# Kernel optimization log

Measured on AMD Instinct MI355X. Metric: run time of the kernel, lower is better.

Reference implementation:

```python
import jax, jax.numpy as jnp
import numpy as np

B, T, D_MODEL = 2, 2048, 2048
N_HEADS, N_KV = 16, 8
HEAD_DIM = D_MODEL // N_HEADS  # 128
EPS = 1e-6


def rmsnorm(x, g):
    # qwen-compatible: compute in fp32, scale by learned weight
    xf = x.astype(jnp.float32)
    var = jnp.mean(xf * xf, axis=-1, keepdims=True)
    return (xf * jax.lax.rsqrt(var + EPS) * g).astype(x.dtype)


def apply_rope(x, cos, sin):
    # x: [b, h, t, d]; cos/sin: [t, d]
    d = x.shape[-1]
    x1, x2 = x[..., : d // 2], x[..., d // 2 :]
    rotated = jnp.concatenate([-x2, x1], axis=-1)
    return x * cos[None, None, :, :] + rotated * sin[None, None, :, :]


def setup_inputs() -> dict:
    key = jax.random.key(0)
    ks = jax.random.split(key, 8)
    x = jax.random.normal(ks[0], (B, T, D_MODEL), dtype=jnp.float32)
    # causal mask: True = masked out
    mask = jnp.triu(jnp.ones((T, T), dtype=bool), k=1)
    # rope tables
    inv_freq = 1.0 / (1e6 ** (np.arange(0, HEAD_DIM, 2, dtype=np.float32) / HEAD_DIM))
    angles = np.arange(T, dtype=np.float32)[:, None] * inv_freq[None, :]  # [T, d/2]
    angles = np.concatenate([angles, angles], axis=1)  # [T, d]
    cos = jnp.asarray(np.cos(angles), dtype=jnp.float32)
    sin = jnp.asarray(np.sin(angles), dtype=jnp.float32)
    s = 0.02
    Wq = jax.random.normal(ks[1], (D_MODEL, D_MODEL), dtype=jnp.float32) * s
    Wk = jax.random.normal(ks[2], (N_KV * HEAD_DIM, D_MODEL), dtype=jnp.float32) * s
    Wv = jax.random.normal(ks[3], (N_KV * HEAD_DIM, D_MODEL), dtype=jnp.float32) * s
    Wo = jax.random.normal(ks[4], (D_MODEL, D_MODEL), dtype=jnp.float32) * s
    bo = jnp.zeros((D_MODEL,), dtype=jnp.float32)
    gq = jnp.ones((HEAD_DIM,), dtype=jnp.float32)
    gk = jnp.ones((HEAD_DIM,), dtype=jnp.float32)
    return {"x": x, "mask": mask, "cos": cos, "sin": sin, "Wq": Wq, "Wk": Wk,
            "Wv": Wv, "Wo": Wo, "bo": bo, "gq": gq, "gk": gk}


def reference(x, mask, cos, sin, Wq, Wk, Wv, Wo, bo, gq, gk):
    b, t, _ = x.shape
    # projections
    q = (x @ Wq.T).reshape(b, t, N_HEADS, HEAD_DIM)
    q = rmsnorm(q, gq).transpose(0, 2, 1, 3)          # [b, H, t, d]
    q = apply_rope(q, cos[:t], sin[:t])
    k = (x @ Wk.T).reshape(b, t, N_KV, HEAD_DIM)
    k = rmsnorm(k, gk).transpose(0, 2, 1, 3)          # [b, G, t, d]
    k = apply_rope(k, cos[:t], sin[:t])
    v = (x @ Wv.T).reshape(b, t, N_KV, HEAD_DIM).transpose(0, 2, 1, 3)
    # GQA broadcast of KV heads
    rep = N_HEADS // N_KV
    k = jnp.repeat(k, rep, axis=1)                    # [b, H, t, d]
    v = jnp.repeat(v, rep, axis=1)
    scores = jnp.einsum("bhqd,bhkd->bhqk", q, k)
    scores = jnp.where(mask[:t, :t][None, None], -jnp.inf, scores)
    attn = jax.nn.softmax(scores / jnp.sqrt(jnp.float32(HEAD_DIM)), axis=-1)
    out = jnp.einsum("bhqk,bhkd->bqhd", attn, v).reshape(b, t, N_HEADS * HEAD_DIM)
    return out @ Wo.T + bo
```

## Files before the change

### kernel.cpp

```cpp
#include <hip/hip_runtime.h>
#include <stdint.h>

#define B_ 2
#define T_ 2048
#define DM 2048
#define NH 16
#define NKV 8
#define HD 128
#define NQKV 4096
#define SC2_ 0.12753102765f

typedef float fx4 __attribute__((ext_vector_type(4)));
typedef __bf16 bfx8 __attribute__((ext_vector_type(8)));
typedef unsigned short u16;
typedef unsigned int u32;

typedef __attribute__((address_space(1))) const void gas_t;
typedef __attribute__((address_space(3))) void las_t;

__device__ __forceinline__ u16 f2bf(float f) {
  u32 u = __float_as_uint(f);
  u = (u + 0x7fffu + ((u >> 16) & 1u)) >> 16;
  return (u16)u;
}

__device__ __forceinline__ u32 cvtpk(float lo, float hi) {
  u32 r;
  asm("v_cvt_pk_bf16_f32 %0, %1, %2" : "=v"(r) : "v"(lo), "v"(hi));
  return r;
}

__device__ __forceinline__ void stage16(const void* g, void* l) {
  __builtin_amdgcn_global_load_lds((gas_t*)(uintptr_t)g, (las_t*)(uintptr_t)l,
                                   16, 0, 0);
}

__global__ void k_cvt(const float* __restrict__ in, u16* __restrict__ out, int n) {
  int i = (blockIdx.x * blockDim.x + threadIdx.x) * 4;
  if (i + 3 < n) {
    float4 v = *(const float4*)(in + i);
    u32 w0 = (u32)f2bf(v.x) | ((u32)f2bf(v.y) << 16);
    u32 w1 = (u32)f2bf(v.z) | ((u32)f2bf(v.w) << 16);
    *(uint2*)(out + i) = make_uint2(w0, w1);
  }
}

__global__ void k_cvtw(const float* __restrict__ wq, const float* __restrict__ wk,
                       const float* __restrict__ wv, const float* __restrict__ wo,
                       u16* __restrict__ out) {
  int i = (blockIdx.x * blockDim.x + threadIdx.x) * 4;
  const float* src;
  int off;
  if (i < 4194304) { src = wq; off = i; }
  else if (i < 6291456) { src = wk; off = i - 4194304; }
  else if (i < 8388608) { src = wv; off = i - 6291456; }
  else { src = wo; off = i - 8388608; }
  float4 v = *(const float4*)(src + off);
  u32 w0 = (u32)f2bf(v.x) | ((u32)f2bf(v.y) << 16);
  u32 w1 = (u32)f2bf(v.z) | ((u32)f2bf(v.w) << 16);
  *(uint2*)(out + i) = make_uint2(w0, w1);
}

__global__ __launch_bounds__(512, 2) void k_gemm256(const u16* __restrict__ A,
                                                    const u16* __restrict__ Bm,
                                                    u16* __restrict__ C,
                                                    int M, int N, int K) {
  __shared__ __align__(16) u16 As[2][2][256 * 32];
  __shared__ __align__(16) u16 Bs[2][2][256 * 32];
  const int nbn = N >> 8;
  const int bm = blockIdx.x / nbn, bn = blockIdx.x % nbn;
  const int tid = threadIdx.x;
  const int w = tid >> 6, lane = tid & 63;
  const int wm = w >> 2, wn = w & 3;
  const int lr = lane & 15, lg = lane >> 4;
  const int cw = (lg ^ ((lr >> 1) & 3)) * 8;
  const u16* Ab = A + (size_t)bm * 256 * K;
  const u16* Bb = Bm + (size_t)bn * 256 * K;
  const int NT = K >> 6;

  auto stage = [&](const u16* gb, u16* region, int tile, int kh) {
#pragma unroll
    for (int i = 0; i < 2; i++) {
      int q = tid + i * 512;
      int row = q >> 2, ch = q & 3;
      int sc = ch ^ ((row >> 1) & 3);
      stage16(gb + (size_t)row * K + tile * 64 + kh * 32 + sc * 8, region + q * 8);
    }
  };

  fx4 acc[8][4];
  const fx4 zero4 = {0.f, 0.f, 0.f, 0.f};
#pragma unroll
  for (int m = 0; m < 8; m++)
#pragma unroll
    for (int n = 0; n < 4; n++) acc[m][n] = zero4;

  stage(Ab, &As[0][0][0], 0, 0);
  stage(Bb, &Bs[0][0][0], 0, 0);
  stage(Ab, &As[0][1][0], 0, 1);
  stage(Bb, &Bs[0][1][0], 0, 1);
  stage(Ab, &As[1][0][0], 1, 0);
  stage(Bb, &Bs[1][0][0], 1, 0);
  asm volatile("s_waitcnt vmcnt(4)" ::: "memory");
  __builtin_amdgcn_s_barrier();

  const int arow = (wm * 128 + lr) * 32;
  const int brow = (wn * 64 + lr) * 32;
  bfx8 af[8], bf[4];

#pragma unroll 1
  for (int t = 0; t < NT; t++) {
    const u16* A0 = &As[t & 1][0][0];
    const u16* A1 = &As[t & 1][1][0];
    const u16* B0 = &Bs[t & 1][0][0];
    const u16* B1 = &Bs[t & 1][1][0];
    const int p1 = (t + 1) & 1, p2 = t & 1;

#pragma unroll
    for (int mi = 0; mi < 8; mi++) af[mi] = *(const bfx8*)(A0 + arow + mi * 512 + cw);
#pragma unroll
    for (int n = 0; n < 4; n++) bf[n] = *(const bfx8*)(B0 + brow + n * 512 + cw);
    if (t + 1 < NT) {
      stage(Ab, &As[p1][1][0], t + 1, 1);
      stage(Bb, &Bs[p1][1][0], t + 1, 1);
    }
    __builtin_amdgcn_s_barrier();
    asm volatile("s_waitcnt lgkmcnt(0)" ::: "memory");
    __builtin_amdgcn_sched_barrier(0);
    __builtin_amdgcn_s_setprio(1);
#pragma unroll
    for (int mi = 0; mi < 8; mi++)
#pragma unroll
      for (int n = 0; n < 4; n++)
        acc[mi][n] = __builtin_amdgcn_mfma_f32_16x16x32_bf16(af[mi], bf[n], acc[mi][n], 0, 0, 0);
    __builtin_amdgcn_s_setprio(0);
    __builtin_amdgcn_s_barrier();

#pragma unroll
    for (int mi = 0; mi < 8; mi++) af[mi] = *(const bfx8*)(A1 + arow + mi * 512 + cw);
#pragma unroll
    for (int n = 0; n < 4; n++) bf[n] = *(const bfx8*)(B1 + brow + n * 512 + cw);
    if (t + 2 < NT) {
      stage(Ab, &As[p2][0][0], t + 2, 0);
      stage(Bb, &Bs[p2][0][0], t + 2, 0);
    }
    __builtin_amdgcn_s_barrier();
    asm volatile("s_waitcnt lgkmcnt(0)" ::: "memory");
    __builtin_amdgcn_sched_barrier(0);
    __builtin_amdgcn_s_setprio(1);
#pragma unroll
    for (int mi = 0; mi < 8; mi++)
#pragma unroll
      for (int n = 0; n < 4; n++)
        acc[mi][n] = __builtin_amdgcn_mfma_f32_16x16x32_bf16(af[mi], bf[n], acc[mi][n], 0, 0, 0);
    __builtin_amdgcn_s_setprio(0);
    if (t + 2 < NT) {
      asm volatile("s_waitcnt vmcnt(4)" ::: "memory");
    } else {
      asm volatile("s_waitcnt vmcnt(0)" ::: "memory");
    }
    __builtin_amdgcn_s_barrier();
  }

  const int r0 = bm * 256 + wm * 128, c0 = bn * 256 + wn * 64;
#pragma unroll
  for (int m = 0; m < 8; m++) {
#pragma unroll
    for (int n = 0; n < 4; n++) {
      int c = c0 + n * 16 + lr;
#pragma unroll
      for (int i = 0; i < 4; i++)
        C[(size_t)(r0 + m * 16 + lg * 4 + i) * N + c] = f2bf(acc[m][n][i]);
    }
  }
}

__global__ __launch_bounds__(256, 2) void k_gemmo(const u16* __restrict__ A,
                                                  const u16* __restrict__ Bm,
                                                  float* __restrict__ C,
                                                  const float* __restrict__ bias,
                                                  int M, int N, int K) {
  __shared__ __align__(16) u16 As[2][2][128 * 32];
  __shared__ __align__(16) u16 Bs[2][2][128 * 32];
  const int nbn = N >> 7;
  const int bm = blockIdx.x / nbn, bn = blockIdx.x % nbn;
  const int tid = threadIdx.x;
  const int w = tid >> 6, lane = tid & 63;
  const int wm = w >> 1, wn = w & 1;
  const int lr = lane & 15, lg = lane >> 4;
  const int cw = (lg ^ ((lr >> 1) & 3)) * 8;
  const u16* Ab = A + (size_t)bm * 128 * K;
  const u16* Bb = Bm + (size_t)bn * 128 * K;
  const int NT = K >> 6;

  auto stage = [&](const u16* gb, u16* region, int tile, int kh) {
#pragma unroll
    for (int i = 0; i < 2; i++) {
      int q = tid + i * 256;
      int row = q >> 2, ch = q & 3;
      int sc = ch ^ ((row >> 1) & 3);
      stage16(gb + (size_t)row * K + tile * 64 + kh * 32 + sc * 8, region + q * 8);
    }
  };

  fx4 acc[4][4];
  const fx4 zero4 = {0.f, 0.f, 0.f, 0.f};
#pragma unroll
  for (int m = 0; m < 4; m++)
#pragma unroll
    for (int n = 0; n < 4; n++) acc[m][n] = zero4;

  stage(Ab, &As[0][0][0], 0, 0);
  stage(Bb, &Bs[0][0][0], 0, 0);
  stage(Ab, &As[0][1][0], 0, 1);
  stage(Bb, &Bs[0][1][0], 0, 1);
  stage(Ab, &As[1][0][0], 1, 0);
  stage(Bb, &Bs[1][0][0], 1, 0);
  asm volatile("s_waitcnt vmcnt(4)" ::: "memory");
  __builtin_amdgcn_s_barrier();

  const int arow = (wm * 64 + lr) * 32;
  const int brow = (wn * 64 + lr) * 32;
  bfx8 af[4], bf[4];

#pragma unroll 1
  for (int t = 0; t < NT; t++) {
    const u16* A0 = &As[t & 1][0][0];
    const u16* A1 = &As[t & 1][1][0];
    const u16* B0 = &Bs[t & 1][0][0];
    const u16* B1 = &Bs[t & 1][1][0];
    const int p1 = (t + 1) & 1, p2 = t & 1;

#pragma unroll
    for (int mi = 0; mi < 4; mi++) af[mi] = *(const bfx8*)(A0 + arow + mi * 512 + cw);
#pragma unroll
    for (int n = 0; n < 4; n++) bf[n] = *(const bfx8*)(B0 + brow + n * 512 + cw);
    if (t + 1 < NT) {
      stage(Ab, &As[p1][1][0], t + 1, 1);
      stage(Bb, &Bs[p1][1][0], t + 1, 1);
    }
    __builtin_amdgcn_s_barrier();
    asm volatile("s_waitcnt lgkmcnt(0)" ::: "memory");
    __builtin_amdgcn_sched_barrier(0);
    __builtin_amdgcn_s_setprio(1);
#pragma unroll
    for (int mi = 0; mi < 4; mi++)
#pragma unroll
      for (int n = 0; n < 4; n++)
        acc[mi][n] = __builtin_amdgcn_mfma_f32_16x16x32_bf16(af[mi], bf[n], acc[mi][n], 0, 0, 0);
    __builtin_amdgcn_s_setprio(0);
    __builtin_amdgcn_s_barrier();

#pragma unroll
    for (int mi = 0; mi < 4; mi++) af[mi] = *(const bfx8*)(A1 + arow + mi * 512 + cw);
#pragma unroll
    for (int n = 0; n < 4; n++) bf[n] = *(const bfx8*)(B1 + brow + n * 512 + cw);
    if (t + 2 < NT) {
      stage(Ab, &As[p2][0][0], t + 2, 0);
      stage(Bb, &Bs[p2][0][0], t + 2, 0);
    }
    __builtin_amdgcn_s_barrier();
    asm volatile("s_waitcnt lgkmcnt(0)" ::: "memory");
    __builtin_amdgcn_sched_barrier(0);
    __builtin_amdgcn_s_setprio(1);
#pragma unroll
    for (int mi = 0; mi < 4; mi++)
#pragma unroll
      for (int n = 0; n < 4; n++)
        acc[mi][n] = __builtin_amdgcn_mfma_f32_16x16x32_bf16(af[mi], bf[n], acc[mi][n], 0, 0, 0);
    __builtin_amdgcn_s_setprio(0);
    if (t + 2 < NT) {
      asm volatile("s_waitcnt vmcnt(4)" ::: "memory");
    } else {
      asm volatile("s_waitcnt vmcnt(0)" ::: "memory");
    }
    __builtin_amdgcn_s_barrier();
  }

  const int r0 = bm * 128 + wm * 64, c0 = bn * 128 + wn * 64;
#pragma unroll
  for (int m = 0; m < 4; m++) {
#pragma unroll
    for (int n = 0; n < 4; n++) {
      int c = c0 + n * 16 + lr;
#pragma unroll
      for (int i = 0; i < 4; i++)
        C[(size_t)(r0 + m * 16 + lg * 4 + i) * N + c] = acc[m][n][i] + bias[c];
    }
  }
}

__global__ __launch_bounds__(256) void k_qkpost(const u16* __restrict__ qkv,
                                                const float* __restrict__ cosp,
                                                const float* __restrict__ sinp,
                                                const float* __restrict__ gq,
                                                const float* __restrict__ gk,
                                                u16* __restrict__ Qo,
                                                u16* __restrict__ Ko) {
  int bi = blockIdx.x;
  int hh = bi % 24;
  int t64 = (bi / 24) % 32;
  int b = bi / 768;
  int tid = threadIdx.x;
  int j = tid >> 2, p = tid & 3;
  int t = t64 * 64 + j;
  bool isq = hh < 16;
  int colbase = isq ? hh * 128 : 2048 + (hh - 16) * 128;
  const u16* src = qkv + ((size_t)(b * T_ + t)) * NQKV + colbase + p * 32;

  float xv[32];
#pragma unroll
  for (int c = 0; c < 4; c++) {
    uint4 raw = *(const uint4*)(src + c * 8);
    u32 wd[4] = {raw.x, raw.y, raw.z, raw.w};
#pragma unroll
    for (int q2 = 0; q2 < 4; q2++) {
      xv[c * 8 + q2 * 2 + 0] = __uint_as_float(wd[q2] << 16);
      xv[c * 8 + q2 * 2 + 1] = __uint_as_float(wd[q2] & 0xffff0000u);
    }
  }
  float ss = 0.f;
#pragma unroll
  for (int i = 0; i < 32; i++) ss += xv[i] * xv[i];
  ss += __shfl_xor(ss, 1);
  ss += __shfl_xor(ss, 2);
  float rinv = rsqrtf(ss * (1.0f / 128.0f) + 1e-6f);
  const float* g = isq ? gq : gk;
  const float* cr = cosp + (size_t)t * 128 + p * 32;
  const float* sr = sinp + (size_t)t * 128 + p * 32;

  float ov[32];
#pragma unroll
  for (int i = 0; i < 32; i++) {
    float y = xv[i] * rinv * g[p * 32 + i];
    float oth = __shfl_xor(y, 2);
    float rot = (p < 2) ? -oth : oth;
    ov[i] = y * cr[i] + rot * sr[i];
  }

  uint4 pk[4];
#pragma unroll
  for (int c = 0; c < 4; c++) {
    u32 wd[4];
#pragma unroll
    for (int q2 = 0; q2 < 4; q2++)
      wd[q2] = (u32)f2bf(ov[c * 8 + q2 * 2]) | ((u32)f2bf(ov[c * 8 + q2 * 2 + 1]) << 16);
    pk[c] = make_uint4(wd[0], wd[1], wd[2], wd[3]);
  }

  if (isq) {
    u16* dst = Qo + (((size_t)(b * NH + hh)) * T_ + t) * HD + p * 32;
#pragma unroll
    for (int c = 0; c < 4; c++) *(uint4*)(dst + c * 8) = pk[c];
  } else {
    int hk = hh - 16;
    u16* dstrow = Ko + (((size_t)(b * NKV + hk)) * T_ + t) * HD;
#pragma unroll
    for (int c = 0; c < 4; c++) {
      int C = p * 4 + c;
      int Cs = C ^ (t & 7);
      *(uint4*)(dstrow + Cs * 8) = pk[c];
    }
  }
}

__global__ __launch_bounds__(256) void k_vtr(const u16* __restrict__ qkv,
                                             u16* __restrict__ vt) {
  __shared__ __align__(16) u16 sm[128 * 64];
  int bi = blockIdx.x;
  int hv = bi & 7;
  int t64 = (bi >> 3) & 31;
  int b = bi >> 8;
  int tid = threadIdx.x;
#pragma unroll
  for (int it = 0; it < 4; it++) {
    int idx = tid + it * 256;
    int tok = idx >> 4, c = idx & 15;
    uint4 raw = *(const uint4*)(qkv + ((size_t)(b * T_ + t64 * 64 + tok)) * NQKV +
                                3072 + hv * 128 + c * 8);
    u32 wd[4] = {raw.x, raw.y, raw.z, raw.w};
#pragma unroll
    for (int q2 = 0; q2 < 4; q2++) {
      sm[(c * 8 + q2 * 2 + 0) * 64 + tok] = (u16)(wd[q2] & 0xffffu);
      sm[(c * 8 + q2 * 2 + 1) * 64 + tok] = (u16)(wd[q2] >> 16);
    }
  }
  __syncthreads();
  int d = tid >> 1, half = tid & 1;
  size_t rowb = (((size_t)(b * NKV + hv)) * HD + d) * T_ + t64 * 64;
#pragma unroll
  for (int c = 0; c < 4; c++) {
    int cg = half * 4 + c;
    int cs = cg ^ (d & 7);
    u32 wd[4];
#pragma unroll
    for (int q2 = 0; q2 < 4; q2++) {
      u32 lo = sm[d * 64 + half * 32 + c * 8 + 2 * q2];
      u32 hi = sm[d * 64 + half * 32 + c * 8 + 2 * q2 + 1];
      wd[q2] = lo | (hi << 16);
    }
    *(uint4*)(vt + rowb + cs * 8) = make_uint4(wd[0], wd[1], wd[2], wd[3]);
  }
}

__global__ __launch_bounds__(512, 4) void k_attn(const u16* __restrict__ Qg,
                                                 const u16* __restrict__ Kg,
                                                 const u16* __restrict__ Vg,
                                                 u16* __restrict__ Og) {
  __shared__ __align__(16) u16 Ks[2][64 * 128];
  __shared__ __align__(16) u16 Vs[2][128 * 64];
  __shared__ __align__(16) u16 Ps[8][16 * 64];
  const int bi = blockIdx.x;
  const int zr = bi & 15, h = (bi >> 4) & 15, b = bi >> 8;
  const int z = b ? (15 - zr) : zr;
  const int hkv = h >> 1;
  const int tid = threadIdx.x, w = tid >> 6, lane = tid & 63;
  const int lr = lane & 15, lg = lane >> 4;
  const int zt = (w < 4) ? z : (31 - z);
  const int qr0 = zt * 64 + (w & 3) * 16;
  const int qrow = qr0 + lr;
  const int nch = 32 - z;
  const int myl = zt + 1;

  const u16* kb = Kg + ((size_t)(b * NKV + hkv)) * T_ * HD;
  const u16* vb = Vg + ((size_t)(b * NKV + hkv)) * HD * T_;
  u16* pw = &Ps[w][0];
  const fx4 zero4 = {0.f, 0.f, 0.f, 0.f};

  auto stageKV = [&](int buf, int kv0) {
    u16* Kd = &Ks[buf][0];
    u16* Vd = &Vs[buf][0];
#pragma unroll
    for (int it = 0; it < 2; it++) {
      int r = it * 32 + (tid >> 4);
      stage16(kb + (size_t)(kv0 + r) * HD + (tid & 15) * 8, Kd + it * 4096 + tid * 8);
      int d = it * 64 + (tid >> 3);
      stage16(vb + (size_t)d * T_ + kv0 + (tid & 7) * 8, Vd + it * 4096 + tid * 8);
    }
  };

  const u16* qbase = Qg + (((size_t)(b * NH + h)) * T_ + qrow) * HD;
  bfx8 qf[4];
#pragma unroll
  for (int kk = 0; kk < 4; kk++) qf[kk] = *(const bfx8*)(qbase + kk * 32 + lg * 8);

  fx4 o[8];
#pragma unroll
  for (int nf = 0; nf < 8; nf++) o[nf] = zero4;
  float l_i = 0.f;

  stageKV(0, 0);
  asm volatile("s_waitcnt vmcnt(0)" ::: "memory");
  __builtin_amdgcn_s_barrier();
  int cur = 0;

#pragma unroll 1
  for (int ch = 0; ch < nch; ch++) {
    if (ch + 1 < nch) {
      stageKV(cur ^ 1, (ch + 1) * 64);
      asm volatile("s_waitcnt vmcnt(4)" ::: "memory");
    } else {
      asm volatile("s_waitcnt vmcnt(0)" ::: "memory");
    }
    __builtin_amdgcn_s_barrier();

    if (ch < myl) {
      const u16* Kd = &Ks[cur][0];
      const u16* Vd = &Vs[cur][0];
      const int kv0 = ch * 64;
      const bool diag = (ch == zt);

      fx4 sa[4];
#pragma unroll
      for (int n = 0; n < 4; n++) sa[n] = zero4;
      __builtin_amdgcn_s_setprio(1);
#pragma unroll
      for (int n = 0; n < 4; n++) {
        const int kvl = n * 16 + lr;
        const u16* krow = Kd + kvl * 128;
#pragma unroll
        for (int kk = 0; kk < 4; kk++) {
          int cs = (kk * 4 + lg) ^ (kvl & 7);
          bfx8 kf = *(const bfx8*)(krow + cs * 8);
          sa[n] = __builtin_amdgcn_mfma_f32_16x16x32_bf16(kf, qf[kk], sa[n], 0, 0, 0);
        }
      }
      __builtin_amdgcn_s_setprio(0);

#pragma unroll
      for (int n = 0; n < 4; n++) {
        float p0 = exp2f(sa[n][0] * SC2_);
        float p1 = exp2f(sa[n][1] * SC2_);
        float p2 = exp2f(sa[n][2] * SC2_);
        float p3 = exp2f(sa[n][3] * SC2_);
        if (diag) {
          int kvg = kv0 + n * 16 + 4 * lg;
          p0 = (kvg + 0 > qrow) ? 0.f : p0;
          p1 = (kvg + 1 > qrow) ? 0.f : p1;
          p2 = (kvg + 2 > qrow) ? 0.f : p2;
          p3 = (kvg + 3 > qrow) ? 0.f : p3;
        }
        l_i += (p0 + p1) + (p2 + p3);
        u32 w0 = cvtpk(p0, p1);
        u32 w1 = cvtpk(p2, p3);
        int c = 2 * n + (lg >> 1);
        int cs = c ^ (lr & 7);
        *(uint2*)(pw + lr * 64 + cs * 8 + 4 * (lg & 1)) = make_uint2(w0, w1);
      }
      asm volatile("s_waitcnt lgkmcnt(0)" ::: "memory");
      __builtin_amdgcn_sched_barrier(0);

      bfx8 pa[2];
#pragma unroll
      for (int ks = 0; ks < 2; ks++) {
        int cp = (4 * ks + lg) ^ (lr & 7);
        pa[ks] = *(const bfx8*)(pw + lr * 64 + cp * 8);
      }
      __builtin_amdgcn_s_setprio(1);
#pragma unroll
      for (int nf = 0; nf < 8; nf++) {
        int d = nf * 16 + lr;
        const u16* vrow = Vd + d * 64;
#pragma unroll
        for (int ks = 0; ks < 2; ks++) {
          int cv = (4 * ks + lg) ^ (d & 7);
          bfx8 vf = *(const bfx8*)(vrow + cv * 8);
          o[nf] = __builtin_amdgcn_mfma_f32_16x16x32_bf16(pa[ks], vf, o[nf], 0, 0, 0);
        }
      }
      __builtin_amdgcn_s_setprio(0);
    }
    __builtin_amdgcn_s_barrier();
    cur ^= 1;
  }

  float lt = l_i + __shfl_xor(l_i, 16);
  lt += __shfl_xor(lt, 32);
  float inv[4];
#pragma unroll
  for (int i = 0; i < 4; i++) inv[i] = 1.0f / __shfl(lt, 4 * lg + i);
  u16* ob = Og + ((size_t)(b * T_ + qr0)) * DM + h * HD;
#pragma unroll
  for (int nf = 0; nf < 8; nf++)
#pragma unroll
    for (int i = 0; i < 4; i++)
      ob[(size_t)(4 * lg + i) * DM + nf * 16 + lr] = f2bf(o[nf][i] * inv[i]);
}

extern "C" void kernel_launch(void* const* d_in, const int* in_sizes, int n_in,
                              void* d_out, int out_size, void* d_ws, size_t ws_size,
                              hipStream_t stream) {
  const float* x = (const float*)d_in[0];
  const float* cosp = (const float*)d_in[2];
  const float* sinp = (const float*)d_in[3];
  const float* Wq = (const float*)d_in[4];
  const float* Wk = (const float*)d_in[5];
  const float* Wv = (const float*)d_in[6];
  const float* Wo = (const float*)d_in[7];
  const float* bo = (const float*)d_in[8];
  const float* gq = (const float*)d_in[9];
  const float* gk = (const float*)d_in[10];

  char* ws = (char*)d_ws;
  u16* xbf  = (u16*)(ws + 0);
  u16* wqkv = (u16*)(ws + 16777216);
  u16* wo   = (u16*)(ws + 33554432);
  u16* qkv  = (u16*)(ws + 41943040);
  u16* qb   = (u16*)(ws + 75497472);
  u16* kb   = (u16*)(ws + 92274688);
  u16* vt   = (u16*)(ws + 100663296);
  u16* ab   = (u16*)(ws + 109051904);
  float* out = (float*)d_out;

  k_cvt<<<8192, 256, 0, stream>>>(x, xbf, 8388608);
  k_cvtw<<<12288, 256, 0, stream>>>(Wq, Wk, Wv, Wo, wqkv);

  k_gemm256<<<256, 512, 0, stream>>>(xbf, wqkv, qkv, 4096, 4096, 2048);
  k_qkpost<<<1536, 256, 0, stream>>>(qkv, cosp, sinp, gq, gk, qb, kb);
  k_vtr<<<512, 256, 0, stream>>>(qkv, vt);
  k_attn<<<512, 512, 0, stream>>>(qb, kb, vt, ab);
  k_gemmo<<<512, 256, 0, stream>>>(ab, wo, out, bo, 4096, 2048, 2048);
}
```

Measured before the change: 230.1 us.

## Process two 16-row query subtiles per wave in attention, halving block size

The attention kernel now runs 4 waves per block instead of 8, and each wave handles 32 query rows as two 16-row subtiles. Each K and V fragment read from LDS therefore feeds two MFMAs, halving LDS fragment reads per unit of compute. The cost is more registers per wave (two sets of Q fragments, output accumulators and score tiles), fewer waves to hide latency, and each thread issuing twice as many KV staging loads. The launch bounds change to 256 threads with a minimum of 2 blocks per SM.

```diff
diff --git a/kernel.cpp b/kernel.cpp
--- a/kernel.cpp
+++ b/kernel.cpp
@@ -403,51 +403,54 @@
   }
 }
 
-__global__ __launch_bounds__(512, 4) void k_attn(const u16* __restrict__ Qg,
+__global__ __launch_bounds__(256, 2) void k_attn(const u16* __restrict__ Qg,
                                                  const u16* __restrict__ Kg,
                                                  const u16* __restrict__ Vg,
                                                  u16* __restrict__ Og) {
   __shared__ __align__(16) u16 Ks[2][64 * 128];
   __shared__ __align__(16) u16 Vs[2][128 * 64];
-  __shared__ __align__(16) u16 Ps[8][16 * 64];
+  __shared__ __align__(16) u16 Ps[4][2][16 * 64];
   const int bi = blockIdx.x;
   const int zr = bi & 15, h = (bi >> 4) & 15, b = bi >> 8;
   const int z = b ? (15 - zr) : zr;
   const int hkv = h >> 1;
   const int tid = threadIdx.x, w = tid >> 6, lane = tid & 63;
   const int lr = lane & 15, lg = lane >> 4;
-  const int zt = (w < 4) ? z : (31 - z);
-  const int qr0 = zt * 64 + (w & 3) * 16;
-  const int qrow = qr0 + lr;
+  const int zt = (w < 2) ? z : (31 - z);
+  const int qr0 = zt * 64 + (w & 1) * 32;
   const int nch = 32 - z;
   const int myl = zt + 1;
 
   const u16* kb = Kg + ((size_t)(b * NKV + hkv)) * T_ * HD;
   const u16* vb = Vg + ((size_t)(b * NKV + hkv)) * HD * T_;
-  u16* pw = &Ps[w][0];
   const fx4 zero4 = {0.f, 0.f, 0.f, 0.f};
 
   auto stageKV = [&](int buf, int kv0) {
     u16* Kd = &Ks[buf][0];
     u16* Vd = &Vs[buf][0];
 #pragma unroll
-    for (int it = 0; it < 2; it++) {
-      int r = it * 32 + (tid >> 4);
-      stage16(kb + (size_t)(kv0 + r) * HD + (tid & 15) * 8, Kd + it * 4096 + tid * 8);
-      int d = it * 64 + (tid >> 3);
-      stage16(vb + (size_t)d * T_ + kv0 + (tid & 7) * 8, Vd + it * 4096 + tid * 8);
+    for (int it = 0; it < 4; it++) {
+      int r = it * 16 + (tid >> 4);
+      stage16(kb + (size_t)(kv0 + r) * HD + (tid & 15) * 8, Kd + it * 2048 + tid * 8);
+      int d = it * 32 + (tid >> 3);
+      stage16(vb + (size_t)d * T_ + kv0 + (tid & 7) * 8, Vd + it * 2048 + tid * 8);
     }
   };
 
-  const u16* qbase = Qg + (((size_t)(b * NH + h)) * T_ + qrow) * HD;
-  bfx8 qf[4];
-#pragma unroll
-  for (int kk = 0; kk < 4; kk++) qf[kk] = *(const bfx8*)(qbase + kk * 32 + lg * 8);
-
-  fx4 o[8];
-#pragma unroll
-  for (int nf = 0; nf < 8; nf++) o[nf] = zero4;
-  float l_i = 0.f;
+  bfx8 qf[2][4];
+#pragma unroll
+  for (int s = 0; s < 2; s++) {
+    const u16* qbase = Qg + (((size_t)(b * NH + h)) * T_ + qr0 + s * 16 + lr) * HD;
+#pragma unroll
+    for (int kk = 0; kk < 4; kk++) qf[s][kk] = *(const bfx8*)(qbase + kk * 32 + lg * 8);
+  }
+
+  fx4 o[2][8];
+#pragma unroll
+  for (int s = 0; s < 2; s++)
+#pragma unroll
+    for (int nf = 0; nf < 8; nf++) o[s][nf] = zero4;
+  float l_i[2] = {0.f, 0.f};
 
   stageKV(0, 0);
   asm volatile("s_waitcnt vmcnt(0)" ::: "memory");
@@ -458,7 +461,7 @@
   for (int ch = 0; ch < nch; ch++) {
     if (ch + 1 < nch) {
       stageKV(cur ^ 1, (ch + 1) * 64);
-      asm volatile("s_waitcnt vmcnt(4)" ::: "memory");
+      asm volatile("s_waitcnt vmcnt(8)" ::: "memory");
     } else {
       asm volatile("s_waitcnt vmcnt(0)" ::: "memory");
     }
@@ -470,9 +473,11 @@
       const int kv0 = ch * 64;
       const bool diag = (ch == zt);
 
-      fx4 sa[4];
-#pragma unroll
-      for (int n = 0; n < 4; n++) sa[n] = zero4;
+      fx4 sa[2][4];
+#pragma unroll
+      for (int s = 0; s < 2; s++)
+#pragma unroll
+        for (int n = 0; n < 4; n++) sa[s][n] = zero4;
       __builtin_amdgcn_s_setprio(1);
 #pragma unroll
       for (int n = 0; n < 4; n++) {
@@ -482,40 +487,48 @@
         for (int kk = 0; kk < 4; kk++) {
           int cs = (kk * 4 + lg) ^ (kvl & 7);
           bfx8 kf = *(const bfx8*)(krow + cs * 8);
-          sa[n] = __builtin_amdgcn_mfma_f32_16x16x32_bf16(kf, qf[kk], sa[n], 0, 0, 0);
+          sa[0][n] = __builtin_amdgcn_mfma_f32_16x16x32_bf16(kf, qf[0][kk], sa[0][n], 0, 0, 0);
+          sa[1][n] = __builtin_amdgcn_mfma_f32_16x16x32_bf16(kf, qf[1][kk], sa[1][n], 0, 0, 0);
         }
       }
       __builtin_amdgcn_s_setprio(0);
 
 #pragma unroll
-      for (int n = 0; n < 4; n++) {
-        float p0 = exp2f(sa[n][0] * SC2_);
-        float p1 = exp2f(sa[n][1] * SC2_);
-        float p2 = exp2f(sa[n][2] * SC2_);
-        float p3 = exp2f(sa[n][3] * SC2_);
-        if (diag) {
-          int kvg = kv0 + n * 16 + 4 * lg;
-          p0 = (kvg + 0 > qrow) ? 0.f : p0;
-          p1 = (kvg + 1 > qrow) ? 0.f : p1;
-          p2 = (kvg + 2 > qrow) ? 0.f : p2;
-          p3 = (kvg + 3 > qrow) ? 0.f : p3;
+      for (int s = 0; s < 2; s++) {
+        const int qrow = qr0 + s * 16 + lr;
+        u16* pw = &Ps[w][s][0];
+#pragma unroll
+        for (int n = 0; n < 4; n++) {
+          float p0 = exp2f(sa[s][n][0] * SC2_);
+          float p1 = exp2f(sa[s][n][1] * SC2_);
+          float p2 = exp2f(sa[s][n][2] * SC2_);
+          float p3 = exp2f(sa[s][n][3] * SC2_);
+          if (diag) {
+            int kvg = kv0 + n * 16 + 4 * lg;
+            p0 = (kvg + 0 > qrow) ? 0.f : p0;
+            p1 = (kvg + 1 > qrow) ? 0.f : p1;
+            p2 = (kvg + 2 > qrow) ? 0.f : p2;
+            p3 = (kvg + 3 > qrow) ? 0.f : p3;
+          }
+          l_i[s] += (p0 + p1) + (p2 + p3);
+          u32 w0 = cvtpk(p0, p1);
+          u32 w1 = cvtpk(p2, p3);
+          int c = 2 * n + (lg >> 1);
+          int cs = c ^ (lr & 7);
+          *(uint2*)(pw + lr * 64 + cs * 8 + 4 * (lg & 1)) = make_uint2(w0, w1);
         }
-        l_i += (p0 + p1) + (p2 + p3);
-        u32 w0 = cvtpk(p0, p1);
-        u32 w1 = cvtpk(p2, p3);
-        int c = 2 * n + (lg >> 1);
-        int cs = c ^ (lr & 7);
-        *(uint2*)(pw + lr * 64 + cs * 8 + 4 * (lg & 1)) = make_uint2(w0, w1);
       }
       asm volatile("s_waitcnt lgkmcnt(0)" ::: "memory");
       __builtin_amdgcn_sched_barrier(0);
 
-      bfx8 pa[2];
-#pragma unroll
-      for (int ks = 0; ks < 2; ks++) {
-        int cp = (4 * ks + lg) ^ (lr & 7);
-        pa[ks] = *(const bfx8*)(pw + lr * 64 + cp * 8);
-      }
+      bfx8 pa[2][2];
+#pragma unroll
+      for (int s = 0; s < 2; s++)
+#pragma unroll
+        for (int ks = 0; ks < 2; ks++) {
+          int cp = (4 * ks + lg) ^ (lr & 7);
+          pa[s][ks] = *(const bfx8*)(&Ps[w][s][0] + lr * 64 + cp * 8);
+        }
       __builtin_amdgcn_s_setprio(1);
 #pragma unroll
       for (int nf = 0; nf < 8; nf++) {
@@ -525,7 +538,8 @@
         for (int ks = 0; ks < 2; ks++) {
           int cv = (4 * ks + lg) ^ (d & 7);
           bfx8 vf = *(const bfx8*)(vrow + cv * 8);
-          o[nf] = __builtin_amdgcn_mfma_f32_16x16x32_bf16(pa[ks], vf, o[nf], 0, 0, 0);
+          o[0][nf] = __builtin_amdgcn_mfma_f32_16x16x32_bf16(pa[0][ks], vf, o[0][nf], 0, 0, 0);
+          o[1][nf] = __builtin_amdgcn_mfma_f32_16x16x32_bf16(pa[1][ks], vf, o[1][nf], 0, 0, 0);
         }
       }
       __builtin_amdgcn_s_setprio(0);
@@ -534,17 +548,20 @@
     cur ^= 1;
   }
 
-  float lt = l_i + __shfl_xor(l_i, 16);
-  lt += __shfl_xor(lt, 32);
-  float inv[4];
-#pragma unroll
-  for (int i = 0; i < 4; i++) inv[i] = 1.0f / __shfl(lt, 4 * lg + i);
-  u16* ob = Og + ((size_t)(b * T_ + qr0)) * DM + h * HD;
-#pragma unroll
-  for (int nf = 0; nf < 8; nf++)
-#pragma unroll
-    for (int i = 0; i < 4; i++)
-      ob[(size_t)(4 * lg + i) * DM + nf * 16 + lr] = f2bf(o[nf][i] * inv[i]);
+#pragma unroll
+  for (int s = 0; s < 2; s++) {
+    float lt = l_i[s] + __shfl_xor(l_i[s], 16);
+    lt += __shfl_xor(lt, 32);
+    float inv[4];
+#pragma unroll
+    for (int i = 0; i < 4; i++) inv[i] = 1.0f / __shfl(lt, 4 * lg + i);
+    u16* ob = Og + ((size_t)(b * T_ + qr0 + s * 16)) * DM + h * HD;
+#pragma unroll
+    for (int nf = 0; nf < 8; nf++)
+#pragma unroll
+      for (int i = 0; i < 4; i++)
+        ob[(size_t)(4 * lg + i) * DM + nf * 16 + lr] = f2bf(o[s][nf][i] * inv[i]);
+  }
 }
 
 extern "C" void kernel_launch(void* const* d_in, const int* in_sizes, int n_in,
@@ -578,6 +595,6 @@
   k_gemm256<<<256, 512, 0, stream>>>(xbf, wqkv, qkv, 4096, 4096, 2048);
   k_qkpost<<<1536, 256, 0, stream>>>(qkv, cosp, sinp, gq, gk, qb, kb);
   k_vtr<<<512, 256, 0, stream>>>(qkv, vt);
-  k_attn<<<512, 512, 0, stream>>>(qb, kb, vt, ab);
+  k_attn<<<512, 256, 0, stream>>>(qb, kb, vt, ab);
   k_gemmo<<<512, 256, 0, stream>>>(ab, wo, out, bo, 4096, 2048, 2048);
 }
```

New measurement: 245.4 us. +6.6%, slower.

## Simplify QKV GEMM to single-stage double buffering with 32-wide K tiles

Applied to the files above, without the earlier changes.

Replaces the QKV projection GEMM's split-half, 4-region LDS pipeline (64-wide K tiles, each staged in two 32-wide halves) with a plain double buffer of 32-wide K tiles. A and B staging are merged into one call, and LDS use per block is halved. The aim is less shared-memory pressure and simpler control flow. In exchange the global prefetch lead drops to one tile, so each load has only one tile of MFMA work to hide behind, and there are two barriers per 32-wide step.

```diff
diff --git a/kernel.cpp b/kernel.cpp
--- a/kernel.cpp
+++ b/kernel.cpp
@@ -65,8 +65,8 @@
                                                     const u16* __restrict__ Bm,
                                                     u16* __restrict__ C,
                                                     int M, int N, int K) {
-  __shared__ __align__(16) u16 As[2][2][256 * 32];
-  __shared__ __align__(16) u16 Bs[2][2][256 * 32];
+  __shared__ __align__(16) u16 As[2][256 * 32];
+  __shared__ __align__(16) u16 Bs[2][256 * 32];
   const int nbn = N >> 8;
   const int bm = blockIdx.x / nbn, bn = blockIdx.x % nbn;
   const int tid = threadIdx.x;
@@ -76,15 +76,18 @@
   const int cw = (lg ^ ((lr >> 1) & 3)) * 8;
   const u16* Ab = A + (size_t)bm * 256 * K;
   const u16* Bb = Bm + (size_t)bn * 256 * K;
-  const int NT = K >> 6;
-
-  auto stage = [&](const u16* gb, u16* region, int tile, int kh) {
+  const int NT = K >> 5;
+
+  auto stage = [&](int buf, int tile) {
+    u16* Ad = &As[buf][0];
+    u16* Bd = &Bs[buf][0];
 #pragma unroll
     for (int i = 0; i < 2; i++) {
       int q = tid + i * 512;
       int row = q >> 2, ch = q & 3;
       int sc = ch ^ ((row >> 1) & 3);
-      stage16(gb + (size_t)row * K + tile * 64 + kh * 32 + sc * 8, region + q * 8);
+      stage16(Ab + (size_t)row * K + tile * 32 + sc * 8, Ad + q * 8);
+      stage16(Bb + (size_t)row * K + tile * 32 + sc * 8, Bd + q * 8);
     }
   };
 
@@ -95,13 +98,8 @@
 #pragma unroll
     for (int n = 0; n < 4; n++) acc[m][n] = zero4;
 
-  stage(Ab, &As[0][0][0], 0, 0);
-  stage(Bb, &Bs[0][0][0], 0, 0);
-  stage(Ab, &As[0][1][0], 0, 1);
-  stage(Bb, &Bs[0][1][0], 0, 1);
-  stage(Ab, &As[1][0][0], 1, 0);
-  stage(Bb, &Bs[1][0][0], 1, 0);
-  asm volatile("s_waitcnt vmcnt(4)" ::: "memory");
+  stage(0, 0);
+  asm volatile("s_waitcnt vmcnt(0)" ::: "memory");
   __builtin_amdgcn_s_barrier();
 
   const int arow = (wm * 128 + lr) * 32;
@@ -110,21 +108,21 @@
 
 #pragma unroll 1
   for (int t = 0; t < NT; t++) {
-    const u16* A0 = &As[t & 1][0][0];
-    const u16* A1 = &As[t & 1][1][0];
-    const u16* B0 = &Bs[t & 1][0][0];
-    const u16* B1 = &Bs[t & 1][1][0];
-    const int p1 = (t + 1) & 1, p2 = t & 1;
-
+    const int cur = t & 1;
+    if (t + 1 < NT) {
+      stage(cur ^ 1, t + 1);
+      asm volatile("s_waitcnt vmcnt(4)" ::: "memory");
+    } else {
+      asm volatile("s_waitcnt vmcnt(0)" ::: "memory");
+    }
+    __builtin_amdgcn_s_barrier();
+
+    const u16* A0 = &As[cur][0];
+    const u16* B0 = &Bs[cur][0];
 #pragma unroll
     for (int mi = 0; mi < 8; mi++) af[mi] = *(const bfx8*)(A0 + arow + mi * 512 + cw);
 #pragma unroll
     for (int n = 0; n < 4; n++) bf[n] = *(const bfx8*)(B0 + brow + n * 512 + cw);
-    if (t + 1 < NT) {
-      stage(Ab, &As[p1][1][0], t + 1, 1);
-      stage(Bb, &Bs[p1][1][0], t + 1, 1);
-    }
-    __builtin_amdgcn_s_barrier();
     asm volatile("s_waitcnt lgkmcnt(0)" ::: "memory");
     __builtin_amdgcn_sched_barrier(0);
     __builtin_amdgcn_s_setprio(1);
@@ -134,31 +132,6 @@
       for (int n = 0; n < 4; n++)
         acc[mi][n] = __builtin_amdgcn_mfma_f32_16x16x32_bf16(af[mi], bf[n], acc[mi][n], 0, 0, 0);
     __builtin_amdgcn_s_setprio(0);
-    __builtin_amdgcn_s_barrier();
-
-#pragma unroll
-    for (int mi = 0; mi < 8; mi++) af[mi] = *(const bfx8*)(A1 + arow + mi * 512 + cw);
-#pragma unroll
-    for (int n = 0; n < 4; n++) bf[n] = *(const bfx8*)(B1 + brow + n * 512 + cw);
-    if (t + 2 < NT) {
-      stage(Ab, &As[p2][0][0], t + 2, 0);
-      stage(Bb, &Bs[p2][0][0], t + 2, 0);
-    }
-    __builtin_amdgcn_s_barrier();
-    asm volatile("s_waitcnt lgkmcnt(0)" ::: "memory");
-    __builtin_amdgcn_sched_barrier(0);
-    __builtin_amdgcn_s_setprio(1);
-#pragma unroll
-    for (int mi = 0; mi < 8; mi++)
-#pragma unroll
-      for (int n = 0; n < 4; n++)
-        acc[mi][n] = __builtin_amdgcn_mfma_f32_16x16x32_bf16(af[mi], bf[n], acc[mi][n], 0, 0, 0);
-    __builtin_amdgcn_s_setprio(0);
-    if (t + 2 < NT) {
-      asm volatile("s_waitcnt vmcnt(4)" ::: "memory");
-    } else {
-      asm volatile("s_waitcnt vmcnt(0)" ::: "memory");
-    }
     __builtin_amdgcn_s_barrier();
   }
 
```

Result: no change. 231.8 us (+0.7%).
